# Kernel optimization log

Hardware: AMD Instinct MI355X
Metric: run time of the kernel (lower is better)

The kernel has to match this reference:

```python
import jax, jax.numpy as jnp
import numpy as np
import math

SIZE = 64
SCALE = math.sqrt(SIZE)
EPS = 1e-12  # torch F.normalize default eps

def l2_normalize(x, axis):
    n = jnp.linalg.norm(x, ord=2, axis=axis, keepdims=True)
    return x / jnp.maximum(n, EPS)

def setup_inputs() -> dict:
    key = jax.random.key(0)
    k1, k2, k3 = jax.random.split(key, 3)
    n, l, s, d, v = 8, 2048, 2048, SIZE, SIZE
    return {
        "query": jax.random.normal(k1, (n, l, d), dtype=jnp.float32),
        "key": jax.random.normal(k2, (n, s, d), dtype=jnp.float32),
        "value": jax.random.normal(k3, (n, s, v), dtype=jnp.float32),
        "mask": jnp.ones((n, l, s), dtype=bool),
    }

def reference(query, key, value, mask):
    # rank-3 query path with normalize=True (cosine attention)
    q = l2_normalize(query, 2)
    k = l2_normalize(key, 2)
    score = jnp.einsum('nlk,nsk->nls', q, k) / SCALE
    score = jnp.where(mask, score, -jnp.inf)
    score = jax.nn.softmax(score, axis=2)  # [n, l, s]
    # equivalent to (score.unsqueeze(3) * value.unsqueeze(1)).sum(2)
    output_value = jnp.einsum('nls,nsv->nlv', score, value)
    return (output_value, score)
```

## Files before the change

kernel.cpp:

```cpp
#include <hip/hip_runtime.h>
#include <hip/hip_bf16.h>
#include <math.h>


typedef __bf16 bf16x8 __attribute__((ext_vector_type(8)));
typedef __bf16 bf16x4 __attribute__((ext_vector_type(4)));
typedef float f32x4 __attribute__((ext_vector_type(4)));

#define NB 8
#define LL 2048
#define SS 2048
#define DD 64
#define MWORDS 64
#define PM_BLOCKS 2048
#define NORM_BLOCKS ((NB * LL * 2) / 4)
#define VT_BLOCKS (NB * (SS / 64))

__global__ __launch_bounds__(256) void prep_all(const float* __restrict__ q,
                                                const float* __restrict__ k,
                                                const float* __restrict__ v,
                                                const int* __restrict__ mask,
                                                __bf16* __restrict__ Qb,
                                                __bf16* __restrict__ Kb,
                                                __bf16* __restrict__ Vt,
                                                unsigned* __restrict__ Mb) {
  __shared__ __bf16 tile[64][72];
  const int bid = blockIdx.x;
  const int t = threadIdx.x;

  if (bid < PM_BLOCKS) {
    const int lane = t & 63;
    const size_t total = (size_t)NB * LL * SS;
    const size_t stride = (size_t)PM_BLOCKS * 256;
    for (size_t i = (size_t)bid * 256 + t; i < total; i += stride) {
      int m = mask[i];
      unsigned long long b = __ballot(m != 0);
      if ((lane & 31) == 0) Mb[i >> 5] = (unsigned)(b >> (lane & 32));
    }
  } else if (bid < PM_BLOCKS + NORM_BLOCKS) {
    const int nb = bid - PM_BLOCKS;
    const int w = t >> 6, lane = t & 63;
    const int r = nb * 4 + w;
    const float* src;
    __bf16* dst;
    float extra;
    if (r < NB * LL) {
      src = q + (size_t)r * DD;
      dst = Qb + (size_t)r * DD;
      extra = 0.125f;
    } else {
      int rk = r - NB * LL;
      src = k + (size_t)rk * DD;
      dst = Kb + (size_t)rk * DD;
      extra = 1.0f;
    }
    float x = src[lane];
    float ss = x * x;
    ss += __shfl_xor(ss, 1);
    ss += __shfl_xor(ss, 2);
    ss += __shfl_xor(ss, 4);
    ss += __shfl_xor(ss, 8);
    ss += __shfl_xor(ss, 16);
    ss += __shfl_xor(ss, 32);
    float nrm = sqrtf(ss);
    float sc = extra / fmaxf(nrm, 1e-12f);
    dst[lane] = (__bf16)(x * sc);
  } else {
    const int vb = bid - PM_BLOCKS - NORM_BLOCKS;
    const int n = vb >> 5;
    const int s0 = (vb & 31) * 64;
#pragma unroll
    for (int it = 0; it < 4; ++it) {
      int idx = t + it * 256;
      int s = idx >> 4, c = idx & 15;
      float4 f = *(const float4*)(v + ((size_t)(n * SS + s0 + s)) * DD + c * 4);
      tile[s][c * 4 + 0] = (__bf16)f.x;
      tile[s][c * 4 + 1] = (__bf16)f.y;
      tile[s][c * 4 + 2] = (__bf16)f.z;
      tile[s][c * 4 + 3] = (__bf16)f.w;
    }
    __syncthreads();
#pragma unroll
    for (int it = 0; it < 4; ++it) {
      int idx = t + it * 256;
      int vv = idx >> 4, c = idx & 15;
      bf16x4 o;
      o[0] = tile[c * 4 + 0][vv];
      o[1] = tile[c * 4 + 1][vv];
      o[2] = tile[c * 4 + 2][vv];
      o[3] = tile[c * 4 + 3][vv];
      *(bf16x4*)(Vt + ((size_t)(n * DD + vv)) * SS + s0 + c * 4) = o;
    }
  }
}

__global__ __launch_bounds__(512, 4) void attn_main(const __bf16* __restrict__ Qb,
                                                    const __bf16* __restrict__ Kb,
                                                    const __bf16* __restrict__ Vt,
                                                    const unsigned* __restrict__ Mb,
                                                    float* __restrict__ out_val,
                                                    float* __restrict__ out_score) {
  __shared__ __bf16 e_lds[2][16][136];
  __shared__ float rs_lds[8][16];
  __shared__ float acc_red[4][16][17];

  const int id = blockIdx.x;
  const int n = id & 7;
  const int l0 = (id >> 3) * 16;

  const int t = threadIdx.x;
  const int w = t >> 6;
  const int lane = t & 63;
  const int m16 = lane & 15;
  const int quad = lane >> 4;
  const int vg = w & 3;
  const int sh = (w >> 2) * 64;

  const __bf16* qrow = Qb + ((size_t)(n * LL + l0 + m16)) * DD;
  bf16x8 aq0 = *(const bf16x8*)(qrow + quad * 8);
  bf16x8 aq1 = *(const bf16x8*)(qrow + 32 + quad * 8);

  const __bf16* kbase = Kb + (size_t)n * SS * DD;
  const __bf16* vrow = Vt + ((size_t)(n * DD + vg * 16 + m16)) * SS + sh;
  const size_t mrow = ((size_t)(n * LL + l0 + m16)) * SS + w * 16 + quad * 4;
  const int off16 = w * 16 + quad * 4;
  const unsigned* mbits = Mb + ((size_t)(n * LL + l0 + m16)) * MWORDS + (off16 >> 5);
  const int bitoff = off16 & 31;

  f32x4 acc_o = {0.f, 0.f, 0.f, 0.f};
  float rsum = 0.f;
  bf16x4 stash[16];
  unsigned bw0 = mbits[0];
  unsigned bw1 = mbits[4];
  unsigned bw2 = mbits[8];
  unsigned bw3 = mbits[12];

#pragma unroll
  for (int c = 0; c < 16; ++c) {
    const int sc = c * 128;
    const int scol = sc + w * 16 + m16;
    const __bf16* krow = kbase + (size_t)scol * DD;
    bf16x8 kb0 = *(const bf16x8*)(krow + quad * 8);
    bf16x8 kb1 = *(const bf16x8*)(krow + 32 + quad * 8);
    bf16x8 bv0 = *(const bf16x8*)(vrow + sc + quad * 8);
    bf16x8 bv1 = *(const bf16x8*)(vrow + sc + 32 + quad * 8);
    f32x4 acc = {0.f, 0.f, 0.f, 0.f};
    acc = __builtin_amdgcn_mfma_f32_16x16x32_bf16(kb0, aq0, acc, 0, 0, 0);
    acc = __builtin_amdgcn_mfma_f32_16x16x32_bf16(kb1, aq1, acc, 0, 0, 0);
    unsigned bits;
    switch (c & 3) {
      case 0: bits = bw0; if (c + 4 < 16) bw0 = mbits[(c + 4) * 4]; break;
      case 1: bits = bw1; if (c + 4 < 16) bw1 = mbits[(c + 4) * 4]; break;
      case 2: bits = bw2; if (c + 4 < 16) bw2 = mbits[(c + 4) * 4]; break;
      default: bits = bw3; if (c + 4 < 16) bw3 = mbits[(c + 4) * 4]; break;
    }
    const unsigned b4 = (bits >> bitoff) & 0xFu;
    float e0 = (b4 & 1u) ? __expf(acc[0]) : 0.f;
    float e1 = (b4 & 2u) ? __expf(acc[1]) : 0.f;
    float e2 = (b4 & 4u) ? __expf(acc[2]) : 0.f;
    float e3 = (b4 & 8u) ? __expf(acc[3]) : 0.f;
    rsum += (e0 + e1) + (e2 + e3);
    bf16x4 sv;
    sv[0] = (__bf16)e0;
    sv[1] = (__bf16)e1;
    sv[2] = (__bf16)e2;
    sv[3] = (__bf16)e3;
    stash[c] = sv;
    *(bf16x4*)(&e_lds[c & 1][m16][w * 16 + quad * 4]) = sv;
    __syncthreads();
    bf16x8 ae0 = *(const bf16x8*)(&e_lds[c & 1][m16][sh + quad * 8]);
    bf16x8 ae1 = *(const bf16x8*)(&e_lds[c & 1][m16][sh + 32 + quad * 8]);
    acc_o = __builtin_amdgcn_mfma_f32_16x16x32_bf16(ae0, bv0, acc_o, 0, 0, 0);
    acc_o = __builtin_amdgcn_mfma_f32_16x16x32_bf16(ae1, bv1, acc_o, 0, 0, 0);
  }

  rsum += __shfl_xor(rsum, 16);
  rsum += __shfl_xor(rsum, 32);
  if (quad == 0) rs_lds[w][m16] = rsum;
  if (w >= 4) {
#pragma unroll
    for (int r = 0; r < 4; ++r) acc_red[vg][quad * 4 + r][m16] = acc_o[r];
  }
  __syncthreads();

  float tot = 0.f;
#pragma unroll
  for (int ww = 0; ww < 8; ++ww) tot += rs_lds[ww][m16];
  const float inv_s = 1.0f / tot;

  if (w < 4) {
#pragma unroll
    for (int r = 0; r < 4; ++r) {
      const int row = quad * 4 + r;
      float tr = 0.f;
#pragma unroll
      for (int ww = 0; ww < 8; ++ww) tr += rs_lds[ww][row];
      const float o = (acc_o[r] + acc_red[vg][row][m16]) / tr;
      __builtin_nontemporal_store(
          o, out_val + ((size_t)(n * LL + l0 + row)) * DD + vg * 16 + m16);
    }
  }

  float* orow = out_score + mrow;
#pragma unroll
  for (int c = 0; c < 16; ++c) {
    f32x4 o;
    o[0] = (float)stash[c][0] * inv_s;
    o[1] = (float)stash[c][1] * inv_s;
    o[2] = (float)stash[c][2] * inv_s;
    o[3] = (float)stash[c][3] * inv_s;
    __builtin_nontemporal_store(o, (f32x4*)(orow + (size_t)c * 128));
  }
}

extern "C" void kernel_launch(void* const* d_in, const int* in_sizes, int n_in,
                              void* d_out, int out_size, void* d_ws, size_t ws_size,
                              hipStream_t stream) {
  const float* q = (const float*)d_in[0];
  const float* k = (const float*)d_in[1];
  const float* v = (const float*)d_in[2];
  const int* mask = (const int*)d_in[3];

  float* out_val = (float*)d_out;
  float* out_score = out_val + (size_t)NB * LL * DD;

  __bf16* Qb = (__bf16*)d_ws;
  __bf16* Kb = Qb + (size_t)NB * LL * DD;
  __bf16* Vt = Kb + (size_t)NB * SS * DD;
  unsigned* Mb = (unsigned*)(Vt + (size_t)NB * DD * SS);

  prep_all<<<dim3(PM_BLOCKS + NORM_BLOCKS + VT_BLOCKS), dim3(256), 0, stream>>>(
      q, k, v, mask, Qb, Kb, Vt, Mb);
  attn_main<<<dim3((LL / 16) * NB), dim3(512), 0, stream>>>(Qb, Kb, Vt, Mb, out_val, out_score);
}
```

Measured before the change: 333.5 us.

## Split S across 4 waves with two-pass recompute, drop per-chunk LDS barriers

The attention kernel moves from 512 to 256 threads. Each wave now owns a contiguous 512-column slice of S instead of interleaving 16-column chunks. A first pass computes only the row sums; a second pass recomputes QK^T and exp, writes normalized scores directly, and feeds P·V through 16x16x16 bf16 MFMAs from registers, so the per-chunk LDS exchange and __syncthreads disappear. This trades double QK/exp compute and K reloads for removing barriers, the register stash and the bf16 round-trip of scores. Score stores are no longer nontemporal.

```diff
diff --git a/kernel.cpp b/kernel.cpp
--- a/kernel.cpp
+++ b/kernel.cpp
@@ -6,6 +6,7 @@
 typedef __bf16 bf16x8 __attribute__((ext_vector_type(8)));
 typedef __bf16 bf16x4 __attribute__((ext_vector_type(4)));
 typedef float f32x4 __attribute__((ext_vector_type(4)));
+typedef short short4v __attribute__((ext_vector_type(4)));
 
 #define NB 8
 #define LL 2048
@@ -15,6 +16,19 @@
 #define PM_BLOCKS 2048
 #define NORM_BLOCKS ((NB * LL * 2) / 4)
 #define VT_BLOCKS (NB * (SS / 64))
+
+static __device__ __forceinline__ f32x4 pv_mfma16(bf16x4 a, bf16x4 b, f32x4 c) {
+#if __has_builtin(__builtin_amdgcn_mfma_f32_16x16x16bf16_1k)
+  return __builtin_amdgcn_mfma_f32_16x16x16bf16_1k(
+      __builtin_bit_cast(short4v, a), __builtin_bit_cast(short4v, b), c, 0, 0, 0);
+#else
+  f32x4 d;
+  asm("s_nop 1\n\tv_mfma_f32_16x16x16_bf16 %0, %1, %2, %3"
+      : "=v"(d)
+      : "v"(a), "v"(b), "v"(c));
+  return d;
+#endif
+}
 
 __global__ __launch_bounds__(256) void prep_all(const float* __restrict__ q,
                                                 const float* __restrict__ k,
@@ -94,15 +108,14 @@
   }
 }
 
-__global__ __launch_bounds__(512, 4) void attn_main(const __bf16* __restrict__ Qb,
+__global__ __launch_bounds__(256, 4) void attn_main(const __bf16* __restrict__ Qb,
                                                     const __bf16* __restrict__ Kb,
                                                     const __bf16* __restrict__ Vt,
                                                     const unsigned* __restrict__ Mb,
                                                     float* __restrict__ out_val,
                                                     float* __restrict__ out_score) {
-  __shared__ __bf16 e_lds[2][16][136];
-  __shared__ float rs_lds[8][16];
-  __shared__ float acc_red[4][16][17];
+  __shared__ float rs[4][16];
+  __shared__ float red[4][16][66];
 
   const int id = blockIdx.x;
   const int n = id & 7;
@@ -113,103 +126,124 @@
   const int lane = t & 63;
   const int m16 = lane & 15;
   const int quad = lane >> 4;
-  const int vg = w & 3;
-  const int sh = (w >> 2) * 64;
+  const int sbase = w * 512;
 
   const __bf16* qrow = Qb + ((size_t)(n * LL + l0 + m16)) * DD;
   bf16x8 aq0 = *(const bf16x8*)(qrow + quad * 8);
   bf16x8 aq1 = *(const bf16x8*)(qrow + 32 + quad * 8);
 
-  const __bf16* kbase = Kb + (size_t)n * SS * DD;
-  const __bf16* vrow = Vt + ((size_t)(n * DD + vg * 16 + m16)) * SS + sh;
-  const size_t mrow = ((size_t)(n * LL + l0 + m16)) * SS + w * 16 + quad * 4;
-  const int off16 = w * 16 + quad * 4;
-  const unsigned* mbits = Mb + ((size_t)(n * LL + l0 + m16)) * MWORDS + (off16 >> 5);
-  const int bitoff = off16 & 31;
-
-  f32x4 acc_o = {0.f, 0.f, 0.f, 0.f};
+  const __bf16* krow = Kb + (size_t)n * SS * DD + (size_t)(sbase + m16) * DD;
+  const __bf16* vbase = Vt + (size_t)n * DD * SS + sbase + quad * 4;
+  const __bf16* vr0 = vbase + (size_t)(0 * 16 + m16) * SS;
+  const __bf16* vr1 = vbase + (size_t)(1 * 16 + m16) * SS;
+  const __bf16* vr2 = vbase + (size_t)(2 * 16 + m16) * SS;
+  const __bf16* vr3 = vbase + (size_t)(3 * 16 + m16) * SS;
+
+  const unsigned* mrow_bits = Mb + ((size_t)(n * LL + l0 + m16)) * MWORDS + w * 16;
+  unsigned mw[16];
+  {
+    uint4 a = *(const uint4*)(mrow_bits + 0);
+    uint4 b = *(const uint4*)(mrow_bits + 4);
+    uint4 cc = *(const uint4*)(mrow_bits + 8);
+    uint4 d = *(const uint4*)(mrow_bits + 12);
+    mw[0] = a.x;  mw[1] = a.y;  mw[2] = a.z;  mw[3] = a.w;
+    mw[4] = b.x;  mw[5] = b.y;  mw[6] = b.z;  mw[7] = b.w;
+    mw[8] = cc.x; mw[9] = cc.y; mw[10] = cc.z; mw[11] = cc.w;
+    mw[12] = d.x; mw[13] = d.y; mw[14] = d.z; mw[15] = d.w;
+  }
+
   float rsum = 0.f;
-  bf16x4 stash[16];
-  unsigned bw0 = mbits[0];
-  unsigned bw1 = mbits[4];
-  unsigned bw2 = mbits[8];
-  unsigned bw3 = mbits[12];
-
-#pragma unroll
-  for (int c = 0; c < 16; ++c) {
-    const int sc = c * 128;
-    const int scol = sc + w * 16 + m16;
-    const __bf16* krow = kbase + (size_t)scol * DD;
-    bf16x8 kb0 = *(const bf16x8*)(krow + quad * 8);
-    bf16x8 kb1 = *(const bf16x8*)(krow + 32 + quad * 8);
-    bf16x8 bv0 = *(const bf16x8*)(vrow + sc + quad * 8);
-    bf16x8 bv1 = *(const bf16x8*)(vrow + sc + 32 + quad * 8);
+  bf16x8 kp0 = *(const bf16x8*)(krow + quad * 8);
+  bf16x8 kp1 = *(const bf16x8*)(krow + 32 + quad * 8);
+  bf16x8 kq0, kq1;
+#pragma unroll
+  for (int c = 0; c < 32; ++c) {
+    bf16x8 k0 = (c & 1) ? kq0 : kp0;
+    bf16x8 k1 = (c & 1) ? kq1 : kp1;
+    if (c + 1 < 32) {
+      const __bf16* kr = krow + (size_t)((c + 1) * 16) * DD;
+      if (c & 1) {
+        kp0 = *(const bf16x8*)(kr + quad * 8);
+        kp1 = *(const bf16x8*)(kr + 32 + quad * 8);
+      } else {
+        kq0 = *(const bf16x8*)(kr + quad * 8);
+        kq1 = *(const bf16x8*)(kr + 32 + quad * 8);
+      }
+    }
     f32x4 acc = {0.f, 0.f, 0.f, 0.f};
-    acc = __builtin_amdgcn_mfma_f32_16x16x32_bf16(kb0, aq0, acc, 0, 0, 0);
-    acc = __builtin_amdgcn_mfma_f32_16x16x32_bf16(kb1, aq1, acc, 0, 0, 0);
-    unsigned bits;
-    switch (c & 3) {
-      case 0: bits = bw0; if (c + 4 < 16) bw0 = mbits[(c + 4) * 4]; break;
-      case 1: bits = bw1; if (c + 4 < 16) bw1 = mbits[(c + 4) * 4]; break;
-      case 2: bits = bw2; if (c + 4 < 16) bw2 = mbits[(c + 4) * 4]; break;
-      default: bits = bw3; if (c + 4 < 16) bw3 = mbits[(c + 4) * 4]; break;
-    }
-    const unsigned b4 = (bits >> bitoff) & 0xFu;
-    float e0 = (b4 & 1u) ? __expf(acc[0]) : 0.f;
-    float e1 = (b4 & 2u) ? __expf(acc[1]) : 0.f;
-    float e2 = (b4 & 4u) ? __expf(acc[2]) : 0.f;
-    float e3 = (b4 & 8u) ? __expf(acc[3]) : 0.f;
-    rsum += (e0 + e1) + (e2 + e3);
+    acc = __builtin_amdgcn_mfma_f32_16x16x32_bf16(k0, aq0, acc, 0, 0, 0);
+    acc = __builtin_amdgcn_mfma_f32_16x16x32_bf16(k1, aq1, acc, 0, 0, 0);
+    const unsigned b4 = (mw[c >> 1] >> (((c & 1) << 4) + quad * 4)) & 0xFu;
+    rsum += ((b4 & 1u) ? __expf(acc[0]) : 0.f) + ((b4 & 2u) ? __expf(acc[1]) : 0.f) +
+            ((b4 & 4u) ? __expf(acc[2]) : 0.f) + ((b4 & 8u) ? __expf(acc[3]) : 0.f);
+  }
+  rsum += __shfl_xor(rsum, 16);
+  rsum += __shfl_xor(rsum, 32);
+  if (quad == 0) rs[w][m16] = rsum;
+  __syncthreads();
+  const float inv_s = 1.0f / (rs[0][m16] + rs[1][m16] + rs[2][m16] + rs[3][m16]);
+
+  f32x4 acc0 = {0.f, 0.f, 0.f, 0.f};
+  f32x4 acc1 = {0.f, 0.f, 0.f, 0.f};
+  f32x4 acc2 = {0.f, 0.f, 0.f, 0.f};
+  f32x4 acc3 = {0.f, 0.f, 0.f, 0.f};
+  float* orow = out_score + ((size_t)(n * LL + l0 + m16)) * SS + sbase + quad * 4;
+  kp0 = *(const bf16x8*)(krow + quad * 8);
+  kp1 = *(const bf16x8*)(krow + 32 + quad * 8);
+#pragma unroll
+  for (int c = 0; c < 32; ++c) {
+    bf16x8 k0 = (c & 1) ? kq0 : kp0;
+    bf16x8 k1 = (c & 1) ? kq1 : kp1;
+    if (c + 1 < 32) {
+      const __bf16* kr = krow + (size_t)((c + 1) * 16) * DD;
+      if (c & 1) {
+        kp0 = *(const bf16x8*)(kr + quad * 8);
+        kp1 = *(const bf16x8*)(kr + 32 + quad * 8);
+      } else {
+        kq0 = *(const bf16x8*)(kr + quad * 8);
+        kq1 = *(const bf16x8*)(kr + 32 + quad * 8);
+      }
+    }
+    bf16x4 bv0 = *(const bf16x4*)(vr0 + c * 16);
+    bf16x4 bv1 = *(const bf16x4*)(vr1 + c * 16);
+    bf16x4 bv2 = *(const bf16x4*)(vr2 + c * 16);
+    bf16x4 bv3 = *(const bf16x4*)(vr3 + c * 16);
+    f32x4 acc = {0.f, 0.f, 0.f, 0.f};
+    acc = __builtin_amdgcn_mfma_f32_16x16x32_bf16(k0, aq0, acc, 0, 0, 0);
+    acc = __builtin_amdgcn_mfma_f32_16x16x32_bf16(k1, aq1, acc, 0, 0, 0);
+    const unsigned b4 = (mw[c >> 1] >> (((c & 1) << 4) + quad * 4)) & 0xFu;
+    const float e0 = (b4 & 1u) ? __expf(acc[0]) : 0.f;
+    const float e1 = (b4 & 2u) ? __expf(acc[1]) : 0.f;
+    const float e2 = (b4 & 4u) ? __expf(acc[2]) : 0.f;
+    const float e3 = (b4 & 8u) ? __expf(acc[3]) : 0.f;
+    f32x4 o = {e0 * inv_s, e1 * inv_s, e2 * inv_s, e3 * inv_s};
+    *(f32x4*)(orow + (size_t)c * 16) = o;
     bf16x4 sv;
     sv[0] = (__bf16)e0;
     sv[1] = (__bf16)e1;
     sv[2] = (__bf16)e2;
     sv[3] = (__bf16)e3;
-    stash[c] = sv;
-    *(bf16x4*)(&e_lds[c & 1][m16][w * 16 + quad * 4]) = sv;
-    __syncthreads();
-    bf16x8 ae0 = *(const bf16x8*)(&e_lds[c & 1][m16][sh + quad * 8]);
-    bf16x8 ae1 = *(const bf16x8*)(&e_lds[c & 1][m16][sh + 32 + quad * 8]);
-    acc_o = __builtin_amdgcn_mfma_f32_16x16x32_bf16(ae0, bv0, acc_o, 0, 0, 0);
-    acc_o = __builtin_amdgcn_mfma_f32_16x16x32_bf16(ae1, bv1, acc_o, 0, 0, 0);
-  }
-
-  rsum += __shfl_xor(rsum, 16);
-  rsum += __shfl_xor(rsum, 32);
-  if (quad == 0) rs_lds[w][m16] = rsum;
-  if (w >= 4) {
-#pragma unroll
-    for (int r = 0; r < 4; ++r) acc_red[vg][quad * 4 + r][m16] = acc_o[r];
+    acc0 = pv_mfma16(sv, bv0, acc0);
+    acc1 = pv_mfma16(sv, bv1, acc1);
+    acc2 = pv_mfma16(sv, bv2, acc2);
+    acc3 = pv_mfma16(sv, bv3, acc3);
+  }
+
+#pragma unroll
+  for (int r = 0; r < 4; ++r) {
+    red[w][quad * 4 + r][0 * 16 + m16] = acc0[r];
+    red[w][quad * 4 + r][1 * 16 + m16] = acc1[r];
+    red[w][quad * 4 + r][2 * 16 + m16] = acc2[r];
+    red[w][quad * 4 + r][3 * 16 + m16] = acc3[r];
   }
   __syncthreads();
-
-  float tot = 0.f;
-#pragma unroll
-  for (int ww = 0; ww < 8; ++ww) tot += rs_lds[ww][m16];
-  const float inv_s = 1.0f / tot;
-
-  if (w < 4) {
-#pragma unroll
-    for (int r = 0; r < 4; ++r) {
-      const int row = quad * 4 + r;
-      float tr = 0.f;
-#pragma unroll
-      for (int ww = 0; ww < 8; ++ww) tr += rs_lds[ww][row];
-      const float o = (acc_o[r] + acc_red[vg][row][m16]) / tr;
-      __builtin_nontemporal_store(
-          o, out_val + ((size_t)(n * LL + l0 + row)) * DD + vg * 16 + m16);
-    }
-  }
-
-  float* orow = out_score + mrow;
-#pragma unroll
-  for (int c = 0; c < 16; ++c) {
-    f32x4 o;
-    o[0] = (float)stash[c][0] * inv_s;
-    o[1] = (float)stash[c][1] * inv_s;
-    o[2] = (float)stash[c][2] * inv_s;
-    o[3] = (float)stash[c][3] * inv_s;
-    __builtin_nontemporal_store(o, (f32x4*)(orow + (size_t)c * 128));
+#pragma unroll
+  for (int i = 0; i < 4; ++i) {
+    const int flat = i * 256 + t;
+    const int l = flat >> 6, vv = flat & 63;
+    const float s = red[0][l][vv] + red[1][l][vv] + red[2][l][vv] + red[3][l][vv];
+    const float tr = rs[0][l] + rs[1][l] + rs[2][l] + rs[3][l];
+    out_val[((size_t)(n * LL + l0 + l)) * DD + vv] = s / tr;
   }
 }
 
@@ -231,5 +265,5 @@
 
   prep_all<<<dim3(PM_BLOCKS + NORM_BLOCKS + VT_BLOCKS), dim3(256), 0, stream>>>(
       q, k, v, mask, Qb, Kb, Vt, Mb);
-  attn_main<<<dim3((LL / 16) * NB), dim3(512), 0, stream>>>(Qb, Kb, Vt, Mb, out_val, out_score);
-}
+  attn_main<<<dim3((LL / 16) * NB), dim3(256), 0, stream>>>(Qb, Kb, Vt, Mb, out_val, out_score);
+}
```

New measurement: 365.8 us. 9.7% more time.
